# Optimization experiments

Hardware: AMD Instinct MI355X
Metric: run time of the kernel (lower is better)

Reference implementation:

```python
import jax, jax.numpy as jnp
import numpy as np

EMB = 1024
NUM_HEADS = 16


def setup_inputs() -> dict:
    key = jax.random.key(0)
    k_x, k_k, k_q, k_v, k_u, k_b = jax.random.split(key, 6)
    b, s, e = 4, 2048, EMB
    lim = 1.0 / np.sqrt(e)
    return {
        "x": jax.random.normal(k_x, (b, s, e), dtype=jnp.float32),
        "Wk": jax.random.uniform(k_k, (e, e), jnp.float32, -lim, lim),
        "Wq": jax.random.uniform(k_q, (e, e), jnp.float32, -lim, lim),
        "Wv": jax.random.uniform(k_v, (e, e), jnp.float32, -lim, lim),
        "Wu": jax.random.uniform(k_u, (e, e), jnp.float32, -lim, lim),
        "bu": jax.random.uniform(k_b, (e,), jnp.float32, -lim, lim),
    }


def reference(x, Wk, Wq, Wv, Wu, bu):
    b, s, e = x.shape
    h = NUM_HEADS
    d = e // h
    # scale q and k each by emb**(-1/4), as in the original (note: emb, not head_size)
    scale = e ** -0.25
    # project and split heads: (b, h, s, d)
    q = (x @ Wq.T).reshape(b, s, h, d).transpose(0, 2, 1, 3) * scale
    k = (x @ Wk.T).reshape(b, s, h, d).transpose(0, 2, 1, 3) * scale
    v = (x @ Wv.T).reshape(b, s, h, d).transpose(0, 2, 1, 3)
    # attention scores (b, h, s, s)
    dot = jnp.einsum("bhqd,bhkd->bhqk", q, k)
    # causal mask: strictly-upper triangle (offset=1) set to -inf
    causal = jnp.triu(jnp.ones((s, s), dtype=bool), k=1)
    dot = jnp.where(causal[None, None, :, :], -jnp.inf, dot)
    attn = jax.nn.softmax(dot, axis=-1)
    out = jnp.einsum("bhqk,bhkd->bhqd", attn, v)
    out = out.transpose(0, 2, 1, 3).reshape(b, s, e)
    return out @ Wu.T + bu
```

## Files before the change

### kernel.cpp

```cpp
#include <hip/hip_runtime.h>
#include <stdint.h>
#include <math.h>


typedef __attribute__((ext_vector_type(8))) short bf16x8;
typedef __attribute__((ext_vector_type(4))) float f32x4;
typedef __attribute__((ext_vector_type(16))) float f32x16;
typedef __attribute__((ext_vector_type(4))) int i32x4;
typedef __attribute__((ext_vector_type(4))) short s16x4;

#define GLOAD_LDS16(gp, lp)                                                     \
  __builtin_amdgcn_global_load_lds(                                             \
      (__attribute__((address_space(1))) void*)(gp),                            \
      (__attribute__((address_space(3))) void*)(lp), 16, 0, 0)

__device__ __forceinline__ short f2bf(float f) {
  union { float f; uint32_t u; } v; v.f = f;
  uint32_t r = v.u + 0x7FFFu + ((v.u >> 16) & 1u);
  return (short)(r >> 16);
}
__device__ __forceinline__ float bf2f(short s) {
  union { uint32_t u; float f; } v; v.u = ((uint32_t)(uint16_t)s) << 16;
  return v.f;
}
__device__ __forceinline__ short f2bfn(float f) {
  union { __bf16 h; short s; } u; u.h = (__bf16)f; return u.s;
}
__device__ __forceinline__ uint32_t pk2n(float a, float b) {
  union { __bf16 h[2]; uint32_t u; } v;
  v.h[0] = (__bf16)a; v.h[1] = (__bf16)b;
  return v.u;
}

__device__ __forceinline__ void swap32(uint32_t a, uint32_t b, int hi,
                                       uint32_t& out0, uint32_t& out1) {
#if __has_builtin(__builtin_amdgcn_permlane32_swap)
  typedef __attribute__((ext_vector_type(2))) int i32x2;
  i32x2 r = __builtin_amdgcn_permlane32_swap((int)a, (int)b, false, false);
  out0 = (uint32_t)r.x; out1 = (uint32_t)r.y;
#else
  uint32_t ta = (uint32_t)__shfl_xor((int)a, 32);
  uint32_t tb = (uint32_t)__shfl_xor((int)b, 32);
  out0 = hi ? tb : a;
  out1 = hi ? b : ta;
#endif
}

__global__ __launch_bounds__(256) void cast_all_kernel(const float* __restrict__ x,
                                                       const float* __restrict__ w0,
                                                       const float* __restrict__ w1,
                                                       const float* __restrict__ w2,
                                                       const float* __restrict__ w3,
                                                       short* __restrict__ xb,
                                                       short* o0, short* o1, short* o2, short* o3) {
  int bid = blockIdx.x;
  const float* src;
  short* dst;
  int i;
  if (bid < 4096) {
    src = x; dst = xb;
    i = (bid * 256 + threadIdx.x) * 8;
  } else {
    int r = bid - 4096;
    int wsel = r >> 9, blk = r & 511;
    src = (wsel == 0) ? w0 : (wsel == 1) ? w1 : (wsel == 2) ? w2 : w3;
    dst = (wsel == 0) ? o0 : (wsel == 1) ? o1 : (wsel == 2) ? o2 : o3;
    i = (blk * 256 + threadIdx.x) * 8;
  }
  const float4* s = (const float4*)(src + i);
  float4 f0 = s[0], f1 = s[1];
  bf16x8 o;
  o[0] = f2bf(f0.x); o[1] = f2bf(f0.y); o[2] = f2bf(f0.z); o[3] = f2bf(f0.w);
  o[4] = f2bf(f1.x); o[5] = f2bf(f1.y); o[6] = f2bf(f1.z); o[7] = f2bf(f1.w);
  *(bf16x8*)(dst + i) = o;
}

template <int MODE>
__device__ __forceinline__ void gemm_bt_core(short* __restrict__ a_lds,
                                             short* __restrict__ b_lds,
                                             const short* __restrict__ A,
                                             const short* __restrict__ Bm,
                                             short* __restrict__ Cb,
                                             float* __restrict__ Cf,
                                             const float* __restrict__ bias,
                                             int row0, int col0) {
  const float QSCALE = 0.03125f * 1.44269504f;
  const int tid = threadIdx.x;
  const int w = tid >> 6, l = tid & 63;
  const int l15 = l & 15, lhi = l >> 4;
  const int wr = w >> 1, wc = w & 1;

  f32x4 acc[4][4];
#pragma unroll
  for (int m = 0; m < 4; ++m)
#pragma unroll
    for (int n = 0; n < 4; ++n)
      acc[m][n] = (f32x4){0.f, 0.f, 0.f, 0.f};

  const int o2 = tid * 16;
  const int r0 = o2 >> 6;
  const int cbyte = o2 & 63;
  const char* Ab0 = (const char*)A + (size_t)(row0 + r0) * 2048 + cbyte;
  const char* Ab1 = Ab0 + (size_t)64 * 2048;
  const char* Bb0 = (const char*)Bm + (size_t)(col0 + r0) * 2048 + cbyte;
  const char* Bb1 = Bb0 + (size_t)64 * 2048;

#define GSTG(t, buf) do {                                                     \
    GLOAD_LDS16(Ab0 + (size_t)(t) * 64, (char*)a_lds + (buf) * 8192 + o2);    \
    GLOAD_LDS16(Ab1 + (size_t)(t) * 64, (char*)a_lds + (buf) * 8192 + 4096 + o2); \
    GLOAD_LDS16(Bb0 + (size_t)(t) * 64, (char*)b_lds + (buf) * 8192 + o2);    \
    GLOAD_LDS16(Bb1 + (size_t)(t) * 64, (char*)b_lds + (buf) * 8192 + 4096 + o2); \
  } while (0)

  GSTG(0, 0);
  GSTG(1, 1);
  asm volatile("s_waitcnt vmcnt(4)" ::: "memory");
  __builtin_amdgcn_s_barrier();
  __builtin_amdgcn_sched_barrier(0);

  int c = 0, cs = 2;
  for (int kt = 0; kt < 32; ++kt) {
    if (kt + 2 < 32) GSTG(kt + 2, cs);
    const char* ab = (const char*)a_lds + c * 8192;
    const char* bb = (const char*)b_lds + c * 8192;
    bf16x8 af[4], bg[4];
#pragma unroll
    for (int m = 0; m < 4; ++m)
      af[m] = *(const bf16x8*)(ab + (wr * 64 + m * 16 + l15) * 64 + lhi * 16);
#pragma unroll
    for (int n = 0; n < 4; ++n)
      bg[n] = *(const bf16x8*)(bb + (wc * 64 + n * 16 + l15) * 64 + lhi * 16);
#pragma unroll
    for (int m = 0; m < 4; ++m)
#pragma unroll
      for (int n = 0; n < 4; ++n)
        acc[m][n] = __builtin_amdgcn_mfma_f32_16x16x32_bf16(af[m], bg[n], acc[m][n], 0, 0, 0);
    if (kt + 2 < 32) {
      asm volatile("s_waitcnt vmcnt(4)" ::: "memory");
    } else {
      asm volatile("s_waitcnt vmcnt(0)" ::: "memory");
    }
    __builtin_amdgcn_s_barrier();
    __builtin_amdgcn_sched_barrier(0);
    c = (c == 2) ? 0 : c + 1;
    cs = (cs == 2) ? 0 : cs + 1;
  }
#undef GSTG

  if constexpr (MODE == 3) {
#pragma unroll
    for (int m = 0; m < 4; ++m)
#pragma unroll
      for (int n = 0; n < 4; ++n) {
        int colg = col0 + wc * 64 + n * 16 + l15;
#pragma unroll
        for (int r = 0; r < 4; ++r) {
          int rowg = row0 + wr * 64 + m * 16 + lhi * 4 + r;
          Cf[(size_t)rowg * 1024 + colg] = acc[m][n][r] + bias[colg];
        }
      }
  } else {
    const int bidx = row0 >> 11;
    const int hh = (col0 >> 6) + wc;
    const int t_base = ((row0 & 2047) + wr * 64) >> 5;
    const size_t base = ((size_t)(bidx * 16 + hh) * 64 + t_base) * 2048;
    if constexpr (MODE == 2) {
      const size_t c0 = base + (lhi >> 1) * 256 + l15 * 8 + (lhi & 1) * 4;
#pragma unroll
      for (int m = 0; m < 4; ++m)
#pragma unroll
        for (int n = 0; n < 4; ++n) {
          size_t idx = c0 + (size_t)(m >> 1) * 2048 + ((n >> 1) * 2 + (m & 1)) * 512 + (n & 1) * 128;
          s16x4 vv;
#pragma unroll
          for (int r = 0; r < 4; ++r) vv[r] = f2bfn(acc[m][n][r]);
          *(s16x4*)(Cb + idx) = vv;
        }
    } else {
      const size_t c0 = base + (l15 >> 3) * 256 + lhi * 32 + (l15 & 7);
#pragma unroll
      for (int m = 0; m < 4; ++m)
#pragma unroll
        for (int n = 0; n < 4; ++n) {
          size_t idx = c0 + (size_t)(m >> 1) * 2048 + n * 512 + (m & 1) * 128;
#pragma unroll
          for (int r = 0; r < 4; ++r)
            Cb[idx + r * 8] = f2bfn(MODE == 0 ? acc[m][n][r] * QSCALE : acc[m][n][r]);
        }
    }
  }
}

__global__ __launch_bounds__(256) void gemm_qkv_kernel(const short* __restrict__ xb,
                                                       const short* __restrict__ wq,
                                                       const short* __restrict__ wk,
                                                       const short* __restrict__ wv,
                                                       short* qf, short* kf, short* vf) {
  __shared__ short a_lds[3 * 4096];
  __shared__ short b_lds[3 * 4096];
  int f = blockIdx.x;
  int g = f & 7, j = f >> 3;
  int rowb = g * 8 + (j & 7);
  int cz = j >> 3;
  int colb = cz & 7, z = cz >> 3;
  int row0 = rowb * 128, col0 = colb * 128;
  if (z == 0)      gemm_bt_core<0>(a_lds, b_lds, xb, wq, qf, nullptr, nullptr, row0, col0);
  else if (z == 1) gemm_bt_core<1>(a_lds, b_lds, xb, wk, kf, nullptr, nullptr, row0, col0);
  else             gemm_bt_core<2>(a_lds, b_lds, xb, wv, vf, nullptr, nullptr, row0, col0);
}

__global__ __launch_bounds__(256) void gemm_out_kernel(const short* __restrict__ ob,
                                                       const short* __restrict__ wu,
                                                       const float* __restrict__ bias,
                                                       float* __restrict__ out) {
  __shared__ short a_lds[3 * 4096];
  __shared__ short b_lds[3 * 4096];
  int f = blockIdx.x;
  int g = f & 7, j = f >> 3;
  int row0 = (g * 8 + (j & 7)) * 128;
  int col0 = (j >> 3) * 128;
  gemm_bt_core<3>(a_lds, b_lds, ob, wu, nullptr, out, bias, row0, col0);
}

__global__ __launch_bounds__(512) void attn_kernel(const short* __restrict__ qf,
                                                   const short* __restrict__ kf,
                                                   const short* __restrict__ vf,
                                                   short* __restrict__ ob) {
  int bh = blockIdx.x;
  int b = bh >> 4, h = bh & 15;
  int tid = threadIdx.x;
  int wid = tid >> 6, l = tid & 63;
  int l31 = l & 31, hi = l >> 5;
  int pair = blockIdx.y * 4 + (wid >> 1);
  int team = wid & 1;
  int slot = wid >> 1;

  __shared__ float mrg[4][64][34];

  const short* qfb = qf + (size_t)bh * 131072;
  const short* kfb = kf + (size_t)bh * 131072;
  const short* vfb = vf + (size_t)bh * 131072;

  for (int part = 0; part < 2; ++part) {
    int sidx = part ? (63 - pair) : pair;
    int qrow0 = sidx * 32;
    int qg = qrow0 + l31;
    int n = sidx + 1;
    int t0 = team ? (n >> 1) : 0;
    int t1 = team ? n : (n >> 1);

    bf16x8 aq[4];
    {
      const short* qp = qfb + sidx * 2048 + l * 8;
#pragma unroll
      for (int s = 0; s < 4; ++s) aq[s] = *(const bf16x8*)(qp + s * 512);
    }

    f32x16 o_lo = {}, o_hi = {};
    float lsum = 0.f;

    if (t0 < t1) {
      const short* kp = kfb + (size_t)t0 * 2048 + l * 8;
      const short* vp = vfb + (size_t)t0 * 2048 + l * 8;
      bf16x8 kc[4];
#pragma unroll
      for (int s = 0; s < 4; ++s) kc[s] = *(const bf16x8*)(kp + s * 512);

      for (int t = t0; t < t1; ++t) {
        bf16x8 vc[4];
#pragma unroll
        for (int s = 0; s < 4; ++s) vc[s] = *(const bf16x8*)(vp + s * 512);
        vp += 2048;

        f32x16 st = {};
        __builtin_amdgcn_s_setprio(1);
#pragma unroll
        for (int s = 0; s < 4; ++s)
          st = __builtin_amdgcn_mfma_f32_32x32x16_bf16(kc[s], aq[s], st, 0, 0, 0);
        __builtin_amdgcn_s_setprio(0);

        kp += 2048;
        {
          const short* kpc = (t + 1 < t1) ? kp : (kp - 2048);
#pragma unroll
          for (int s = 0; s < 4; ++s) kc[s] = *(const bf16x8*)(kpc + s * 512);
        }

        if (t == sidx) {
#pragma unroll
          for (int r = 0; r < 16; ++r) {
            int kk = qrow0 + (r & 3) + 8 * (r >> 2) + 4 * hi;
            if (kk > qg) st[r] = -INFINITY;
          }
        }

#pragma unroll
        for (int r = 0; r < 16; ++r) st[r] = exp2f(st[r]);

        float sm[8];
#pragma unroll
        for (int r = 0; r < 8; ++r) sm[r] = st[r] + st[r + 8];
#pragma unroll
        for (int r = 0; r < 4; ++r) sm[r] += sm[r + 4];
        lsum += (sm[0] + sm[1]) + (sm[2] + sm[3]);

        uint32_t a0, a2, b1, b3, c0, c2, d1, d3;
        swap32(pk2n(st[0], st[1]),   pk2n(st[4], st[5]),   hi, a0, a2);
        swap32(pk2n(st[2], st[3]),   pk2n(st[6], st[7]),   hi, b1, b3);
        swap32(pk2n(st[8], st[9]),   pk2n(st[12], st[13]), hi, c0, c2);
        swap32(pk2n(st[10], st[11]), pk2n(st[14], st[15]), hi, d1, d3);
        i32x4 u0 = {(int)a0, (int)b1, (int)a2, (int)b3};
        i32x4 u1 = {(int)c0, (int)d1, (int)c2, (int)d3};
        bf16x8 pa0 = __builtin_bit_cast(bf16x8, u0);
        bf16x8 pa1 = __builtin_bit_cast(bf16x8, u1);

        __builtin_amdgcn_s_setprio(1);
        o_lo = __builtin_amdgcn_mfma_f32_32x32x16_bf16(vc[0], pa0, o_lo, 0, 0, 0);
        o_lo = __builtin_amdgcn_mfma_f32_32x32x16_bf16(vc[1], pa1, o_lo, 0, 0, 0);
        o_hi = __builtin_amdgcn_mfma_f32_32x32x16_bf16(vc[2], pa0, o_hi, 0, 0, 0);
        o_hi = __builtin_amdgcn_mfma_f32_32x32x16_bf16(vc[3], pa1, o_hi, 0, 0, 0);
        __builtin_amdgcn_s_setprio(0);
      }
    }

    lsum += __shfl_xor(lsum, 32);

    if (team == 1) {
      float* pp = &mrg[slot][l][0];
#pragma unroll
      for (int r = 0; r < 16; ++r) { pp[r] = o_lo[r]; pp[16 + r] = o_hi[r]; }
      pp[32] = lsum;
    }
    __syncthreads();
    if (team == 0) {
      const float* pp = &mrg[slot][l][0];
      float inv = 1.0f / (lsum + pp[32]);
      short* obase = ob + (size_t)(b * 2048 + qg) * 1024 + h * 64;
#pragma unroll
      for (int g = 0; g < 4; ++g) {
        int d0 = 8 * g + 4 * hi;
        s16x4 v0, v1;
#pragma unroll
        for (int jj = 0; jj < 4; ++jj) {
          v0[jj] = f2bfn((o_lo[4 * g + jj] + pp[4 * g + jj]) * inv);
          v1[jj] = f2bfn((o_hi[4 * g + jj] + pp[16 + 4 * g + jj]) * inv);
        }
        *(s16x4*)(obase + d0) = v0;
        *(s16x4*)(obase + 32 + d0) = v1;
      }
    }
    __syncthreads();
  }
}

extern "C" void kernel_launch(void* const* d_in, const int* in_sizes, int n_in,
                              void* d_out, int out_size, void* d_ws, size_t ws_size,
                              hipStream_t stream) {
  const float* x  = (const float*)d_in[0];
  const float* Wk = (const float*)d_in[1];
  const float* Wq = (const float*)d_in[2];
  const float* Wv = (const float*)d_in[3];
  const float* Wu = (const float*)d_in[4];
  const float* bu = (const float*)d_in[5];
  float* out = (float*)d_out;

  char* ws = (char*)d_ws;
  const size_t MB = 1u << 20;
  short* xb  = (short*)(ws + 0 * MB);
  short* qf  = (short*)(ws + 16 * MB);
  short* kfb = (short*)(ws + 32 * MB);
  short* vfb = (short*)(ws + 48 * MB);
  short* ob  = (short*)(ws + 64 * MB);
  short* wqb = (short*)(ws + 80 * MB);
  short* wkb = (short*)(ws + 82 * MB);
  short* wvb = (short*)(ws + 84 * MB);
  short* wub = (short*)(ws + 86 * MB);

  cast_all_kernel<<<6144, 256, 0, stream>>>(x, Wq, Wk, Wv, Wu, xb, wqb, wkb, wvb, wub);
  gemm_qkv_kernel<<<1536, 256, 0, stream>>>(xb, wqb, wkb, wvb, qf, kfb, vfb);
  attn_kernel<<<dim3(64, 8), 512, 0, stream>>>(qf, kfb, vfb, ob);
  gemm_out_kernel<<<512, 256, 0, stream>>>(ob, wub, bu, out);
}
```

Before: 177.4 us.

## Process 64 query rows per wave pair to reuse K/V tiles across two blocks

Each attention workgroup now has two waves that split the key range, and each wave handles 64 query rows (two 32-row sub-blocks A and B) instead of 32. Every loaded K and V tile is then used for two score and PV MFMA chains, roughly halving K/V global loads per query. The launch changes from 512-thread blocks on an 8-wide grid to 128-thread blocks on a 16-wide grid. The cost is more accumulator registers per wave and fewer waves per block, which may lower occupancy and latency hiding, plus a per-tile branch for the causal diagonal.

```diff
diff --git a/kernel.cpp b/kernel.cpp
--- a/kernel.cpp
+++ b/kernel.cpp
@@ -222,44 +222,45 @@
   gemm_bt_core<3>(a_lds, b_lds, ob, wu, nullptr, out, bias, row0, col0);
 }
 
-__global__ __launch_bounds__(512) void attn_kernel(const short* __restrict__ qf,
+__global__ __launch_bounds__(128) void attn_kernel(const short* __restrict__ qf,
                                                    const short* __restrict__ kf,
                                                    const short* __restrict__ vf,
                                                    short* __restrict__ ob) {
   int bh = blockIdx.x;
   int b = bh >> 4, h = bh & 15;
-  int tid = threadIdx.x;
-  int wid = tid >> 6, l = tid & 63;
+  int j = blockIdx.y;
+  int team = threadIdx.x >> 6;
+  int l = threadIdx.x & 63;
   int l31 = l & 31, hi = l >> 5;
-  int pair = blockIdx.y * 4 + (wid >> 1);
-  int team = wid & 1;
-  int slot = wid >> 1;
-
-  __shared__ float mrg[4][64][34];
+
+  __shared__ float mrg[64][66];
 
   const short* qfb = qf + (size_t)bh * 131072;
   const short* kfb = kf + (size_t)bh * 131072;
   const short* vfb = vf + (size_t)bh * 131072;
 
   for (int part = 0; part < 2; ++part) {
-    int sidx = part ? (63 - pair) : pair;
-    int qrow0 = sidx * 32;
-    int qg = qrow0 + l31;
-    int n = sidx + 1;
+    int sidx = part ? (31 - j) : j;
+    int qgA = sidx * 64 + l31;
+    int qgB = qgA + 32;
+    int n = 2 * sidx + 2;
     int t0 = team ? (n >> 1) : 0;
     int t1 = team ? n : (n >> 1);
 
-    bf16x8 aq[4];
+    bf16x8 aqA[4], aqB[4];
     {
-      const short* qp = qfb + sidx * 2048 + l * 8;
-#pragma unroll
-      for (int s = 0; s < 4; ++s) aq[s] = *(const bf16x8*)(qp + s * 512);
-    }
-
-    f32x16 o_lo = {}, o_hi = {};
-    float lsum = 0.f;
-
-    if (t0 < t1) {
+      const short* qpA = qfb + (size_t)(2 * sidx) * 2048 + l * 8;
+#pragma unroll
+      for (int s = 0; s < 4; ++s) {
+        aqA[s] = *(const bf16x8*)(qpA + s * 512);
+        aqB[s] = *(const bf16x8*)(qpA + 2048 + s * 512);
+      }
+    }
+
+    f32x16 oA_lo = {}, oA_hi = {}, oB_lo = {}, oB_hi = {};
+    float lsA = 0.f, lsB = 0.f;
+
+    {
       const short* kp = kfb + (size_t)t0 * 2048 + l * 8;
       const short* vp = vfb + (size_t)t0 * 2048 + l * 8;
       bf16x8 kc[4];
@@ -272,81 +273,128 @@
         for (int s = 0; s < 4; ++s) vc[s] = *(const bf16x8*)(vp + s * 512);
         vp += 2048;
 
-        f32x16 st = {};
-        __builtin_amdgcn_s_setprio(1);
-#pragma unroll
-        for (int s = 0; s < 4; ++s)
-          st = __builtin_amdgcn_mfma_f32_32x32x16_bf16(kc[s], aq[s], st, 0, 0, 0);
-        __builtin_amdgcn_s_setprio(0);
-
-        kp += 2048;
+        if (t <= 2 * sidx) {
+          f32x16 st = {};
+          __builtin_amdgcn_s_setprio(1);
+#pragma unroll
+          for (int s = 0; s < 4; ++s)
+            st = __builtin_amdgcn_mfma_f32_32x32x16_bf16(kc[s], aqA[s], st, 0, 0, 0);
+          __builtin_amdgcn_s_setprio(0);
+          if (t == 2 * sidx) {
+            int k0 = t * 32;
+#pragma unroll
+            for (int r = 0; r < 16; ++r) {
+              int kk = k0 + (r & 3) + 8 * (r >> 2) + 4 * hi;
+              if (kk > qgA) st[r] = -INFINITY;
+            }
+          }
+#pragma unroll
+          for (int r = 0; r < 16; ++r) st[r] = exp2f(st[r]);
+          float sm[8];
+#pragma unroll
+          for (int r = 0; r < 8; ++r) sm[r] = st[r] + st[r + 8];
+#pragma unroll
+          for (int r = 0; r < 4; ++r) sm[r] += sm[r + 4];
+          lsA += (sm[0] + sm[1]) + (sm[2] + sm[3]);
+          uint32_t a0, a2, b1, b3, c0, c2, d1, d3;
+          swap32(pk2n(st[0], st[1]),   pk2n(st[4], st[5]),   hi, a0, a2);
+          swap32(pk2n(st[2], st[3]),   pk2n(st[6], st[7]),   hi, b1, b3);
+          swap32(pk2n(st[8], st[9]),   pk2n(st[12], st[13]), hi, c0, c2);
+          swap32(pk2n(st[10], st[11]), pk2n(st[14], st[15]), hi, d1, d3);
+          i32x4 u0 = {(int)a0, (int)b1, (int)a2, (int)b3};
+          i32x4 u1 = {(int)c0, (int)d1, (int)c2, (int)d3};
+          bf16x8 pa0 = __builtin_bit_cast(bf16x8, u0);
+          bf16x8 pa1 = __builtin_bit_cast(bf16x8, u1);
+          __builtin_amdgcn_s_setprio(1);
+          oA_lo = __builtin_amdgcn_mfma_f32_32x32x16_bf16(vc[0], pa0, oA_lo, 0, 0, 0);
+          oA_lo = __builtin_amdgcn_mfma_f32_32x32x16_bf16(vc[1], pa1, oA_lo, 0, 0, 0);
+          oA_hi = __builtin_amdgcn_mfma_f32_32x32x16_bf16(vc[2], pa0, oA_hi, 0, 0, 0);
+          oA_hi = __builtin_amdgcn_mfma_f32_32x32x16_bf16(vc[3], pa1, oA_hi, 0, 0, 0);
+          __builtin_amdgcn_s_setprio(0);
+        }
+
         {
-          const short* kpc = (t + 1 < t1) ? kp : (kp - 2048);
-#pragma unroll
-          for (int s = 0; s < 4; ++s) kc[s] = *(const bf16x8*)(kpc + s * 512);
-        }
-
-        if (t == sidx) {
-#pragma unroll
-          for (int r = 0; r < 16; ++r) {
-            int kk = qrow0 + (r & 3) + 8 * (r >> 2) + 4 * hi;
-            if (kk > qg) st[r] = -INFINITY;
+          f32x16 st = {};
+          __builtin_amdgcn_s_setprio(1);
+#pragma unroll
+          for (int s = 0; s < 4; ++s)
+            st = __builtin_amdgcn_mfma_f32_32x32x16_bf16(kc[s], aqB[s], st, 0, 0, 0);
+          __builtin_amdgcn_s_setprio(0);
+          kp += 2048;
+          {
+            const short* kpc = (t + 1 < t1) ? kp : (kp - 2048);
+#pragma unroll
+            for (int s = 0; s < 4; ++s) kc[s] = *(const bf16x8*)(kpc + s * 512);
           }
-        }
-
-#pragma unroll
-        for (int r = 0; r < 16; ++r) st[r] = exp2f(st[r]);
-
-        float sm[8];
-#pragma unroll
-        for (int r = 0; r < 8; ++r) sm[r] = st[r] + st[r + 8];
-#pragma unroll
-        for (int r = 0; r < 4; ++r) sm[r] += sm[r + 4];
-        lsum += (sm[0] + sm[1]) + (sm[2] + sm[3]);
-
-        uint32_t a0, a2, b1, b3, c0, c2, d1, d3;
-        swap32(pk2n(st[0], st[1]),   pk2n(st[4], st[5]),   hi, a0, a2);
-        swap32(pk2n(st[2], st[3]),   pk2n(st[6], st[7]),   hi, b1, b3);
-        swap32(pk2n(st[8], st[9]),   pk2n(st[12], st[13]), hi, c0, c2);
-        swap32(pk2n(st[10], st[11]), pk2n(st[14], st[15]), hi, d1, d3);
-        i32x4 u0 = {(int)a0, (int)b1, (int)a2, (int)b3};
-        i32x4 u1 = {(int)c0, (int)d1, (int)c2, (int)d3};
-        bf16x8 pa0 = __builtin_bit_cast(bf16x8, u0);
-        bf16x8 pa1 = __builtin_bit_cast(bf16x8, u1);
-
-        __builtin_amdgcn_s_setprio(1);
-        o_lo = __builtin_amdgcn_mfma_f32_32x32x16_bf16(vc[0], pa0, o_lo, 0, 0, 0);
-        o_lo = __builtin_amdgcn_mfma_f32_32x32x16_bf16(vc[1], pa1, o_lo, 0, 0, 0);
-        o_hi = __builtin_amdgcn_mfma_f32_32x32x16_bf16(vc[2], pa0, o_hi, 0, 0, 0);
-        o_hi = __builtin_amdgcn_mfma_f32_32x32x16_bf16(vc[3], pa1, o_hi, 0, 0, 0);
-        __builtin_amdgcn_s_setprio(0);
+          if (t == 2 * sidx + 1) {
+            int k0 = t * 32;
+#pragma unroll
+            for (int r = 0; r < 16; ++r) {
+              int kk = k0 + (r & 3) + 8 * (r >> 2) + 4 * hi;
+              if (kk > qgB) st[r] = -INFINITY;
+            }
+          }
+#pragma unroll
+          for (int r = 0; r < 16; ++r) st[r] = exp2f(st[r]);
+          float sm[8];
+#pragma unroll
+          for (int r = 0; r < 8; ++r) sm[r] = st[r] + st[r + 8];
+#pragma unroll
+          for (int r = 0; r < 4; ++r) sm[r] += sm[r + 4];
+          lsB += (sm[0] + sm[1]) + (sm[2] + sm[3]);
+          uint32_t a0, a2, b1, b3, c0, c2, d1, d3;
+          swap32(pk2n(st[0], st[1]),   pk2n(st[4], st[5]),   hi, a0, a2);
+          swap32(pk2n(st[2], st[3]),   pk2n(st[6], st[7]),   hi, b1, b3);
+          swap32(pk2n(st[8], st[9]),   pk2n(st[12], st[13]), hi, c0, c2);
+          swap32(pk2n(st[10], st[11]), pk2n(st[14], st[15]), hi, d1, d3);
+          i32x4 u0 = {(int)a0, (int)b1, (int)a2, (int)b3};
+          i32x4 u1 = {(int)c0, (int)d1, (int)c2, (int)d3};
+          bf16x8 pa0 = __builtin_bit_cast(bf16x8, u0);
+          bf16x8 pa1 = __builtin_bit_cast(bf16x8, u1);
+          __builtin_amdgcn_s_setprio(1);
+          oB_lo = __builtin_amdgcn_mfma_f32_32x32x16_bf16(vc[0], pa0, oB_lo, 0, 0, 0);
+          oB_lo = __builtin_amdgcn_mfma_f32_32x32x16_bf16(vc[1], pa1, oB_lo, 0, 0, 0);
+          oB_hi = __builtin_amdgcn_mfma_f32_32x32x16_bf16(vc[2], pa0, oB_hi, 0, 0, 0);
+          oB_hi = __builtin_amdgcn_mfma_f32_32x32x16_bf16(vc[3], pa1, oB_hi, 0, 0, 0);
+          __builtin_amdgcn_s_setprio(0);
+        }
       }
     }
 
-    lsum += __shfl_xor(lsum, 32);
+    lsA += __shfl_xor(lsA, 32);
+    lsB += __shfl_xor(lsB, 32);
 
     if (team == 1) {
-      float* pp = &mrg[slot][l][0];
-#pragma unroll
-      for (int r = 0; r < 16; ++r) { pp[r] = o_lo[r]; pp[16 + r] = o_hi[r]; }
-      pp[32] = lsum;
+      float* pp = &mrg[l][0];
+#pragma unroll
+      for (int r = 0; r < 16; ++r) {
+        pp[r] = oA_lo[r]; pp[16 + r] = oA_hi[r];
+        pp[32 + r] = oB_lo[r]; pp[48 + r] = oB_hi[r];
+      }
+      pp[64] = lsA; pp[65] = lsB;
     }
     __syncthreads();
     if (team == 0) {
-      const float* pp = &mrg[slot][l][0];
-      float inv = 1.0f / (lsum + pp[32]);
-      short* obase = ob + (size_t)(b * 2048 + qg) * 1024 + h * 64;
+      const float* pp = &mrg[l][0];
+      float invA = 1.0f / (lsA + pp[64]);
+      float invB = 1.0f / (lsB + pp[65]);
+      short* obaseA = ob + (size_t)(b * 2048 + qgA) * 1024 + h * 64;
+      short* obaseB = ob + (size_t)(b * 2048 + qgB) * 1024 + h * 64;
 #pragma unroll
       for (int g = 0; g < 4; ++g) {
         int d0 = 8 * g + 4 * hi;
-        s16x4 v0, v1;
+        s16x4 v0, v1, v2, v3;
 #pragma unroll
         for (int jj = 0; jj < 4; ++jj) {
-          v0[jj] = f2bfn((o_lo[4 * g + jj] + pp[4 * g + jj]) * inv);
-          v1[jj] = f2bfn((o_hi[4 * g + jj] + pp[16 + 4 * g + jj]) * inv);
-        }
-        *(s16x4*)(obase + d0) = v0;
-        *(s16x4*)(obase + 32 + d0) = v1;
+          v0[jj] = f2bfn((oA_lo[4 * g + jj] + pp[4 * g + jj]) * invA);
+          v1[jj] = f2bfn((oA_hi[4 * g + jj] + pp[16 + 4 * g + jj]) * invA);
+          v2[jj] = f2bfn((oB_lo[4 * g + jj] + pp[32 + 4 * g + jj]) * invB);
+          v3[jj] = f2bfn((oB_hi[4 * g + jj] + pp[48 + 4 * g + jj]) * invB);
+        }
+        *(s16x4*)(obaseA + d0) = v0;
+        *(s16x4*)(obaseA + 32 + d0) = v1;
+        *(s16x4*)(obaseB + d0) = v2;
+        *(s16x4*)(obaseB + 32 + d0) = v3;
       }
     }
     __syncthreads();
@@ -378,6 +426,6 @@
 
   cast_all_kernel<<<6144, 256, 0, stream>>>(x, Wq, Wk, Wv, Wu, xb, wqb, wkb, wvb, wub);
   gemm_qkv_kernel<<<1536, 256, 0, stream>>>(xb, wqb, wkb, wvb, qf, kfb, vfb);
-  attn_kernel<<<dim3(64, 8), 512, 0, stream>>>(qf, kfb, vfb, ob);
+  attn_kernel<<<dim3(64, 16), 128, 0, stream>>>(qf, kfb, vfb, ob);
   gemm_out_kernel<<<512, 256, 0, stream>>>(ob, wub, bu, out);
 }
```

Result: slower. 186.7 us (+5.3%).
